# Kernel tuning notes

Measured on AMD Instinct MI355X. Metric: run time of the kernel, lower is better.

The kernel has to match this reference:

```python
import jax, jax.numpy as jnp
import numpy as np
import math

D_MODEL = 1024
HEADS = 16
D_K = D_MODEL // HEADS
D_FF = 2048
EPS = 1e-6
NEG = -1e9


def _layernorm(x, gamma, beta):
    mu = x.mean(axis=-1, keepdims=True)
    var = ((x - mu) ** 2).mean(axis=-1, keepdims=True)
    return gamma * (x - mu) / jnp.sqrt(var + EPS) + beta


def setup_inputs() -> dict:
    key = jax.random.key(0)
    ks = jax.random.split(key, 12)
    B, S = 8, 1024
    s = 0.02
    return {
        "x": jax.random.normal(ks[0], (B, S, D_MODEL), jnp.float32),
        "mask": jnp.ones((B, 1, S), jnp.int32),
        "wq": jax.random.normal(ks[1], (D_MODEL, D_MODEL), jnp.float32) * s,
        "bq": jnp.zeros((D_MODEL,), jnp.float32),
        "wk": jax.random.normal(ks[2], (D_MODEL, D_MODEL), jnp.float32) * s,
        "bk": jnp.zeros((D_MODEL,), jnp.float32),
        "wv": jax.random.normal(ks[3], (D_MODEL, D_MODEL), jnp.float32) * s,
        "bv": jnp.zeros((D_MODEL,), jnp.float32),
        "wo": jax.random.normal(ks[4], (D_MODEL, D_MODEL), jnp.float32) * s,
        "bo": jnp.zeros((D_MODEL,), jnp.float32),
        "w1": jax.random.normal(ks[5], (D_MODEL, D_FF), jnp.float32) * s,
        "b1": jnp.zeros((D_FF,), jnp.float32),
        "w2": jax.random.normal(ks[6], (D_FF, D_MODEL), jnp.float32) * s,
        "b2": jnp.zeros((D_MODEL,), jnp.float32),
        "g1": jnp.ones((D_MODEL,), jnp.float32),
        "be1": jnp.zeros((D_MODEL,), jnp.float32),
        "g2": jnp.ones((D_MODEL,), jnp.float32),
        "be2": jnp.zeros((D_MODEL,), jnp.float32),
    }


def reference(x, mask, wq, bq, wk, bk, wv, bv, wo, bo, w1, b1, w2, b2, g1, be1, g2, be2):
    B, S, _ = x.shape
    # QKV projections, split heads: [B,H,S,d_k]
    q = (x @ wq + bq).reshape(B, S, HEADS, D_K).transpose(0, 2, 1, 3)
    k = (x @ wk + bk).reshape(B, S, HEADS, D_K).transpose(0, 2, 1, 3)
    v = (x @ wv + bv).reshape(B, S, HEADS, D_K).transpose(0, 2, 1, 3)
    scores = jnp.einsum("bhqd,bhkd->bhqk", q, k) / math.sqrt(D_K)
    m = mask[:, None, :, :]  # [B,1,1|S,S] broadcast over heads
    scores = jnp.where(m == 0, NEG, scores)
    attn = jax.nn.softmax(scores, axis=-1)
    out = jnp.einsum("bhqk,bhkd->bhqd", attn, v)
    concat = out.transpose(0, 2, 1, 3).reshape(B, S, D_MODEL)
    attn_out = concat @ wo + bo
    x1 = _layernorm(x + attn_out, g1, be1)
    ff = jax.nn.relu(x1 @ w1 + b1) @ w2 + b2
    return _layernorm(x1 + ff, g2, be2)
```

## Files before the change

### kernel.cpp

```cpp
#include <hip/hip_runtime.h>
#include <stdint.h>

using u16 = unsigned short;
using u32 = unsigned int;
typedef __attribute__((ext_vector_type(4))) float f32x4;
typedef __attribute__((ext_vector_type(8))) short s16x8;

#define LOG2E 1.44269504088896340736f
#define SCL (0.125f * LOG2E)

__device__ __forceinline__ u16 f2b(float f) {
  union { float f; u32 u; } v; v.f = f;
  u32 r = v.u + 0x7fffu + ((v.u >> 16) & 1u);
  return (u16)(r >> 16);
}

__device__ __forceinline__ float b2f(u16 x) {
  union { u32 u; float f; } v; v.u = (u32)x << 16; return v.f;
}

__device__ __forceinline__ u32 pack2(u16 lo, u16 hi) {
  return (u32)lo | ((u32)hi << 16);
}

__device__ __forceinline__ u32 cvtpk(float lo, float hi) {
  u32 r;
  asm("v_cvt_pk_bf16_f32 %0, %1, %2" : "=v"(r) : "v"(lo), "v"(hi));
  return r;
}

__device__ __forceinline__ f32x4 mfma16(s16x8 a, s16x8 b, f32x4 c) {
  return __builtin_amdgcn_mfma_f32_16x16x32_bf16(a, b, c, 0, 0, 0);
}

__device__ __forceinline__ void gload16(const void* g, void* l) {
  __builtin_amdgcn_global_load_lds(
      (const __attribute__((address_space(1))) void*)g,
      (__attribute__((address_space(3))) void*)l, 16, 0, 0);
}

__global__ __launch_bounds__(256) void cvt_bf16(const float* __restrict__ in,
                                                u16* __restrict__ out, int n4) {
  int i = blockIdx.x * 256 + threadIdx.x;
  if (i >= n4) return;
  float4 v = ((const float4*)in)[i];
  uint2 o;
  o.x = pack2(f2b(v.x), f2b(v.y));
  o.y = pack2(f2b(v.z), f2b(v.w));
  ((uint2*)out)[i] = o;
}

__global__ __launch_bounds__(256) void transpose_cvt(const float* __restrict__ in,
                                                     u16* __restrict__ outT,
                                                     int K, int N) {
  __shared__ float t[32][33];
  int n0 = blockIdx.x * 32, k0 = blockIdx.y * 32;
  int tx = threadIdx.x, ty = threadIdx.y;
#pragma unroll
  for (int i = 0; i < 4; i++)
    t[ty + i * 8][tx] = in[(size_t)(k0 + ty + i * 8) * N + n0 + tx];
  __syncthreads();
#pragma unroll
  for (int i = 0; i < 4; i++)
    outT[(size_t)(n0 + ty + i * 8) * K + k0 + tx] = f2b(t[tx][ty + i * 8]);
}

__global__ __launch_bounds__(256) void bias_pack(const float* __restrict__ bq,
                                                 const float* __restrict__ bk,
                                                 const float* __restrict__ bv,
                                                 float* __restrict__ o) {
  int i = blockIdx.x * 256 + threadIdx.x;
  o[i] = (i < 1024) ? bq[i] : (i < 2048) ? bk[i - 1024] : bv[i - 2048];
}

template <int EPI, int BN, int WM, int WN>
__global__ __launch_bounds__(512, 1) void gemm8(const u16* __restrict__ A,
                                                const u16* __restrict__ Bt,
                                                const float* __restrict__ bias,
                                                void* __restrict__ outp,
                                                void* __restrict__ outp2,
                                                int N, int K) {
  constexpr int MI = 256 / (WM * 16);
  constexpr int NJ = BN / (WN * 16);
  constexpr int BB = BN / 128;
  __shared__ u16 As[4][256 * 32];
  __shared__ u16 Bs[4][BN * 32];
  int tid = threadIdx.x;
  int wv = tid >> 6, ln = tid & 63;
  int fr = ln & 15, fg = ln >> 4;
  int wm = wv / WN, wn = wv % WN;

  int x = blockIdx.x & 7;
  int l = blockIdx.x >> 3;
  int m0 = (x * 4 + (l & 3)) * 256;
  int n0 = (l >> 2) * BN;

  auto stageA = [&](int buf, int kt) {
#pragma unroll
    for (int s = 0; s < 2; s++) {
      int idx = s * 512 + tid;
      int row = idx >> 2, ch = idx & 3;
      int sw = (row ^ (row >> 2)) & 3;
      int gcol = kt * 32 + ((ch ^ sw) << 3);
      gload16(A + (size_t)(m0 + row) * K + gcol,
              &As[buf][(size_t)(s * 512 + (wv << 6)) * 8]);
    }
  };
  auto stageB = [&](int buf, int kt) {
#pragma unroll
    for (int s = 0; s < BB; s++) {
      int idx = s * 512 + tid;
      int row = idx >> 2, ch = idx & 3;
      int sw = (row ^ (row >> 2)) & 3;
      int gcol = kt * 32 + ((ch ^ sw) << 3);
      gload16(Bt + (size_t)(n0 + row) * K + gcol,
              &Bs[buf][(size_t)(s * 512 + (wv << 6)) * 8]);
    }
  };

  f32x4 acc[MI][NJ] = {};
  int NT = K >> 5;

#pragma unroll
  for (int tt = 0; tt < 3; ++tt) { stageA(tt, tt); stageB(tt, tt); }

  for (int t = 0; t < NT; ++t) {
    if constexpr (BN == 256) asm volatile("s_waitcnt vmcnt(8)" ::: "memory");
    else                     asm volatile("s_waitcnt vmcnt(6)" ::: "memory");
    __builtin_amdgcn_s_barrier();
    __builtin_amdgcn_sched_barrier(0);

    const u16* Ab = As[t & 3];
    const u16* Bb = Bs[t & 3];
    s16x8 af[MI], bf[NJ];
#pragma unroll
    for (int j = 0; j < NJ; j++) {
      int row = wn * (BN / WN) + j * 16 + fr;
      int sw = (row ^ (row >> 2)) & 3;
      bf[j] = *(const s16x8*)&Bb[row * 32 + ((fg ^ sw) << 3)];
    }
#pragma unroll
    for (int i = 0; i < MI; i++) {
      int row = wm * (256 / WM) + i * 16 + fr;
      int sw = (row ^ (row >> 2)) & 3;
      af[i] = *(const s16x8*)&Ab[row * 32 + ((fg ^ sw) << 3)];
    }

    int tn = (t + 3 < NT) ? t + 3 : NT - 1;
    stageA((t + 3) & 3, tn);
    stageB((t + 3) & 3, tn);

    __builtin_amdgcn_sched_barrier(0);
    __builtin_amdgcn_s_setprio(1);
#pragma unroll
    for (int i = 0; i < MI; i++)
#pragma unroll
      for (int j = 0; j < NJ; j++)
        acc[i][j] = mfma16(af[i], bf[j], acc[i][j]);
    __builtin_amdgcn_s_setprio(0);
    __builtin_amdgcn_sched_barrier(0);
  }

#pragma unroll
  for (int j = 0; j < NJ; j++) {
    int coll = n0 + wn * (BN / WN) + j * 16 + fr;
    float bv = bias[coll];
#pragma unroll
    for (int i = 0; i < MI; i++) {
      int rowbase = m0 + wm * (256 / WM) + i * 16 + fg * 4;
      if (EPI == 4) {
        if (coll < 2048) {
          u16* o = (u16*)outp + (size_t)(coll >> 10) * (8192u * 1024u) + (coll & 1023);
#pragma unroll
          for (int r = 0; r < 4; r++)
            o[(size_t)(rowbase + r) * 1024] = f2b(acc[i][j][r] + bv);
        } else {
          int cv = coll - 2048;
          int b_ = rowbase >> 10, s_ = rowbase & 1023;
          int h_ = cv >> 6, d_ = cv & 63;
          float v0 = acc[i][j][0] + bv, v1 = acc[i][j][1] + bv;
          float v2 = acc[i][j][2] + bv, v3 = acc[i][j][3] + bv;
          uint2 o; o.x = pack2(f2b(v0), f2b(v1)); o.y = pack2(f2b(v2), f2b(v3));
          *(uint2*)((u16*)outp2 + (((size_t)((b_ * 16 + h_) * 64 + d_)) << 10) + s_) = o;
        }
      } else {
#pragma unroll
        for (int r = 0; r < 4; r++) {
          int row = rowbase + r;
          float v = acc[i][j][r] + bv;
          if (EPI == 2) v = v > 0.f ? v : 0.f;
          if (EPI == 1)
            ((float*)outp)[(size_t)row * N + coll] = v;
          else
            ((u16*)outp)[(size_t)row * N + coll] = f2b(v);
        }
      }
    }
  }
}

__global__ __launch_bounds__(256) void attn_fwd(const u16* __restrict__ q,
                                                const u16* __restrict__ k,
                                                const u16* __restrict__ vT,
                                                const int* __restrict__ mask,
                                                u16* __restrict__ ctx) {
  __shared__ u16 Ks[64 * 64];
  __shared__ u16 Vs[2][64 * 64];
  __shared__ u16 Ps[4][32 * 64];
  int tid = threadIdx.x, wv = tid >> 6, ln = tid & 63;
  int fr = ln & 15, fg = ln >> 4;
  int bh = blockIdx.x, b = bh >> 4, h = bh & 15;
  int q0 = blockIdx.y * 128;

  const u16* kbase = k + (size_t)b * 1024 * 1024 + h * 64;
  const u16* vbase = vT + (size_t)bh * 64 * 1024;
#define STAGE_K(kt)                                                           \
  {                                                                           \
    _Pragma("unroll") for (int j = 0; j < 2; j++) {                           \
      int c = wv * 64 + j * 256, cl = c + ln;                                 \
      int rr = cl >> 3, csw = (cl & 7) ^ (rr & 7);                            \
      gload16(kbase + (size_t)((kt) * 64 + rr) * 1024 + csw * 8, Ks + c * 8); \
    }                                                                         \
  }
#define STAGE_V(buf, kt)                                                      \
  {                                                                           \
    _Pragma("unroll") for (int j = 0; j < 2; j++) {                           \
      int c = wv * 64 + j * 256, cl = c + ln;                                 \
      int rr = cl >> 3, csw = (cl & 7) ^ (rr & 7);                            \
      gload16(vbase + (size_t)rr * 1024 + (kt) * 64 + csw * 8,                \
              Vs[buf] + c * 8);                                               \
    }                                                                         \
  }

  STAGE_K(0);
  STAGE_V(0, 0);

  int4 mv0 = *(const int4*)(mask + b * 1024 + tid * 4);
  int ok = (mv0.x != 0) & (mv0.y != 0) & (mv0.z != 0) & (mv0.w != 0);
  int seq_ok = __syncthreads_and(ok);

  s16x8 qf[2][2];
#pragma unroll
  for (int i = 0; i < 2; i++)
#pragma unroll
    for (int ks = 0; ks < 2; ks++) {
      int row = q0 + wv * 32 + i * 16 + fr;
      qf[i][ks] = *(const s16x8*)(q + (size_t)(b * 1024 + row) * 1024 + h * 64 + ks * 32 + fg * 8);
      u32* qw = (u32*)&qf[i][ks];
#pragma unroll
      for (int w = 0; w < 4; w++) {
        union { u32 u; float f; } lo, hi;
        lo.u = qw[w] << 16; hi.u = qw[w] & 0xffff0000u;
        qw[w] = cvtpk(lo.f * SCL, hi.f * SCL);
      }
    }

  s16x8 ones;
#pragma unroll
  for (int j = 0; j < 8; j++) ones[j] = (short)0x3F80;

  f32x4 ao[2][4] = {};
  f32x4 aol[2] = {};
  float mrun[2];
  mrun[0] = mrun[1] = -1e30f;

  int bsrc = (ln & 48) | ((ln >> 2) & 12);

  __syncthreads();

  for (int kt = 0; kt < 16; ++kt) {
    int cur = kt & 1;

    f32x4 st[4][2] = {};
    __builtin_amdgcn_s_setprio(1);
#pragma unroll
    for (int ks = 0; ks < 2; ks++)
#pragma unroll
      for (int jm = 0; jm < 4; jm++) {
        s16x8 kfr = *(const s16x8*)(Ks + (jm * 16 + fr) * 64 + (((ks * 4 + fg) ^ (fr & 7)) << 3));
        st[jm][0] = mfma16(kfr, qf[0][ks], st[jm][0]);
        st[jm][1] = mfma16(kfr, qf[1][ks], st[jm][1]);
      }
    __builtin_amdgcn_s_setprio(0);

    __syncthreads();
    if (kt < 15) {
      STAGE_K(kt + 1);
      STAGE_V(cur ^ 1, kt + 1);
    }

    if (!seq_ok) {
#pragma unroll
      for (int jm = 0; jm < 4; jm++) {
        int4 mv = *(const int4*)(mask + b * 1024 + kt * 64 + jm * 16 + fg * 4);
        float m0 = mv.x == 0 ? -1e9f * SCL : 0.f;
        float m1 = mv.y == 0 ? -1e9f * SCL : 0.f;
        float m2 = mv.z == 0 ? -1e9f * SCL : 0.f;
        float m3 = mv.w == 0 ? -1e9f * SCL : 0.f;
#pragma unroll
        for (int i = 0; i < 2; i++) {
          st[jm][i][0] += m0; st[jm][i][1] += m1;
          st[jm][i][2] += m2; st[jm][i][3] += m3;
        }
      }
    }

    float mx[2];
#pragma unroll
    for (int i = 0; i < 2; i++) {
      float m = fmaxf(fmaxf(st[0][i][0], st[0][i][1]), st[0][i][2]);
      m = fmaxf(fmaxf(m, st[0][i][3]), st[1][i][0]);
      m = fmaxf(fmaxf(m, st[1][i][1]), st[1][i][2]);
      m = fmaxf(fmaxf(m, st[1][i][3]), st[2][i][0]);
      m = fmaxf(fmaxf(m, st[2][i][1]), st[2][i][2]);
      m = fmaxf(fmaxf(m, st[2][i][3]), st[3][i][0]);
      m = fmaxf(fmaxf(m, st[3][i][1]), st[3][i][2]);
      m = fmaxf(m, st[3][i][3]);
      m = fmaxf(m, __shfl_xor(m, 16));
      m = fmaxf(m, __shfl_xor(m, 32));
      mx[i] = m;
    }

    bool need = (mx[0] > mrun[0] + 8.f) || (mx[1] > mrun[1] + 8.f);
    if (__any(need)) {
      float al[2];
#pragma unroll
      for (int i = 0; i < 2; i++) {
        float mnew = fmaxf(mrun[i], mx[i]);
        al[i] = __builtin_exp2f(mrun[i] - mnew);
        mrun[i] = mnew;
      }
#pragma unroll
      for (int io = 0; io < 2; io++) {
        float a0 = __shfl(al[io], bsrc + 0), a1 = __shfl(al[io], bsrc + 1);
        float a2 = __shfl(al[io], bsrc + 2), a3 = __shfl(al[io], bsrc + 3);
        aol[io][0] *= a0; aol[io][1] *= a1; aol[io][2] *= a2; aol[io][3] *= a3;
#pragma unroll
        for (int jd = 0; jd < 4; jd++) {
          ao[io][jd][0] *= a0; ao[io][jd][1] *= a1;
          ao[io][jd][2] *= a2; ao[io][jd][3] *= a3;
        }
      }
    }

#pragma unroll
    for (int i = 0; i < 2; i++)
#pragma unroll
      for (int jm = 0; jm < 4; jm++)
#pragma unroll
        for (int r = 0; r < 4; r++)
          st[jm][i][r] = __builtin_exp2f(st[jm][i][r] - mrun[i]);

    u16* Pw = Ps[wv];
#pragma unroll
    for (int i = 0; i < 2; i++) {
      int qrow = i * 16 + fr;
      int rowoff = qrow * 64;
      int sw = (qrow & 7) << 3;
#pragma unroll
      for (int jm = 0; jm < 4; jm++) {
        uint2 pk;
        pk.x = cvtpk(st[jm][i][0], st[jm][i][1]);
        pk.y = cvtpk(st[jm][i][2], st[jm][i][3]);
        *(uint2*)(Pw + ((rowoff + jm * 16 + fg * 4) ^ sw)) = pk;
      }
    }

    const u16* Vc = Vs[cur];
    __builtin_amdgcn_s_setprio(1);
#pragma unroll
    for (int ks = 0; ks < 2; ks++) {
      int ch = ((ks * 4 + fg) ^ (fr & 7)) << 3;
      s16x8 pa0 = *(const s16x8*)(Pw + fr * 64 + ch);
      s16x8 pa1 = *(const s16x8*)(Pw + (16 + fr) * 64 + ch);
#pragma unroll
      for (int jd = 0; jd < 4; jd++) {
        s16x8 bv = *(const s16x8*)(Vc + (jd * 16 + fr) * 64 + ch);
        ao[0][jd] = mfma16(pa0, bv, ao[0][jd]);
        ao[1][jd] = mfma16(pa1, bv, ao[1][jd]);
      }
      aol[0] = mfma16(pa0, ones, aol[0]);
      aol[1] = mfma16(pa1, ones, aol[1]);
    }
    __builtin_amdgcn_s_setprio(0);

    __syncthreads();
  }

#pragma unroll
  for (int io = 0; io < 2; io++) {
    float i0 = 1.f / aol[io][0], i1 = 1.f / aol[io][1];
    float i2 = 1.f / aol[io][2], i3 = 1.f / aol[io][3];
#pragma unroll
    for (int jd = 0; jd < 4; jd++) {
      int d = jd * 16 + fr;
      int rowb = wv * 32 + io * 16 + fg * 4;
      u16* cb = ctx + (size_t)(b * 1024 + q0 + rowb) * 1024 + h * 64 + d;
      cb[0]    = f2b(ao[io][jd][0] * i0);
      cb[1024] = f2b(ao[io][jd][1] * i1);
      cb[2048] = f2b(ao[io][jd][2] * i2);
      cb[3072] = f2b(ao[io][jd][3] * i3);
    }
  }
#undef STAGE_K
#undef STAGE_V
}

template <bool ABF16, bool BBF16>
__global__ __launch_bounds__(256) void ln_fused(const void* __restrict__ a,
                                                const void* __restrict__ bsrc,
                                                const float* __restrict__ gamma,
                                                const float* __restrict__ beta,
                                                float* __restrict__ outf,
                                                u16* __restrict__ outb) {
  int row = blockIdx.x, tid = threadIdx.x;
  float v0, v1, v2, v3;
  if (ABF16) {
    uint2 va = ((const uint2*)((const u16*)a + (size_t)row * 1024))[tid];
    v0 = b2f((u16)(va.x & 0xffff)); v1 = b2f((u16)(va.x >> 16));
    v2 = b2f((u16)(va.y & 0xffff)); v3 = b2f((u16)(va.y >> 16));
  } else {
    float4 va = ((const float4*)((const float*)a + (size_t)row * 1024))[tid];
    v0 = va.x; v1 = va.y; v2 = va.z; v3 = va.w;
  }
  if (BBF16) {
    uint2 vb = ((const uint2*)((const u16*)bsrc + (size_t)row * 1024))[tid];
    v0 += b2f((u16)(vb.x & 0xffff)); v1 += b2f((u16)(vb.x >> 16));
    v2 += b2f((u16)(vb.y & 0xffff)); v3 += b2f((u16)(vb.y >> 16));
  } else {
    float4 vb = ((const float4*)((const float*)bsrc + (size_t)row * 1024))[tid];
    v0 += vb.x; v1 += vb.y; v2 += vb.z; v3 += vb.w;
  }
  float s = v0 + v1 + v2 + v3;
  float ss = v0 * v0 + v1 * v1 + v2 * v2 + v3 * v3;
#pragma unroll
  for (int m = 1; m < 64; m <<= 1) { s += __shfl_xor(s, m); ss += __shfl_xor(ss, m); }
  __shared__ float rs[8];
  int wv = tid >> 6;
  if ((tid & 63) == 0) { rs[wv] = s; rs[4 + wv] = ss; }
  __syncthreads();
  s = rs[0] + rs[1] + rs[2] + rs[3];
  ss = rs[4] + rs[5] + rs[6] + rs[7];
  float mu = s * (1.f / 1024.f);
  float var = ss * (1.f / 1024.f) - mu * mu;
  float rstd = rsqrtf(var + 1e-6f);
  float4 g4 = ((const float4*)gamma)[tid];
  float4 be4 = ((const float4*)beta)[tid];
  float y0 = g4.x * (v0 - mu) * rstd + be4.x;
  float y1 = g4.y * (v1 - mu) * rstd + be4.y;
  float y2 = g4.z * (v2 - mu) * rstd + be4.z;
  float y3 = g4.w * (v3 - mu) * rstd + be4.w;
  if (outf) {
    float4 o; o.x = y0; o.y = y1; o.z = y2; o.w = y3;
    ((float4*)(outf + (size_t)row * 1024))[tid] = o;
  }
  if (outb) {
    uint2 ob; ob.x = pack2(f2b(y0), f2b(y1)); ob.y = pack2(f2b(y2), f2b(y3));
    ((uint2*)(outb + (size_t)row * 1024))[tid] = ob;
  }
}

extern "C" void kernel_launch(void* const* d_in, const int* in_sizes, int n_in,
                              void* d_out, int out_size, void* d_ws, size_t ws_size,
                              hipStream_t stream) {
  const float* x   = (const float*)d_in[0];
  const int*   msk = (const int*)d_in[1];
  const float* wq  = (const float*)d_in[2];
  const float* bq  = (const float*)d_in[3];
  const float* wk  = (const float*)d_in[4];
  const float* bk  = (const float*)d_in[5];
  const float* wv  = (const float*)d_in[6];
  const float* bv  = (const float*)d_in[7];
  const float* wo  = (const float*)d_in[8];
  const float* bo  = (const float*)d_in[9];
  const float* w1  = (const float*)d_in[10];
  const float* b1  = (const float*)d_in[11];
  const float* w2  = (const float*)d_in[12];
  const float* b2  = (const float*)d_in[13];
  const float* g1  = (const float*)d_in[14];
  const float* be1 = (const float*)d_in[15];
  const float* g2  = (const float*)d_in[16];
  const float* be2 = (const float*)d_in[17];
  float* out = (float*)d_out;
  char* ws = (char*)d_ws;
  const size_t MB = 1u << 20;

  u16* xb  = (u16*)(ws + 0);
  u16* wqt = (u16*)(ws + 16 * MB);
  u16* wkt = (u16*)(ws + 18 * MB);
  u16* wvt = (u16*)(ws + 20 * MB);
  u16* wot = (u16*)(ws + 22 * MB);
  u16* w1t = (u16*)(ws + 24 * MB);
  u16* w2t = (u16*)(ws + 28 * MB);
  u16* qb  = (u16*)(ws + 32 * MB);
  u16* kb  = (u16*)(ws + 48 * MB);
  u16* vT  = (u16*)(ws + 64 * MB);
  u16* ctx = (u16*)(ws + 80 * MB);
  float* bqkv = (float*)(ws + 80 * MB);
  u16* attn_out = (u16*)(ws + 32 * MB);
  u16* x1b = (u16*)(ws + 0);
  u16* hb  = (u16*)(ws + 96 * MB);
  u16* fff = (u16*)(ws + 48 * MB);

  dim3 tb(32, 8);
  cvt_bf16<<<8192, 256, 0, stream>>>(x, xb, 8192 * 1024 / 4);
  transpose_cvt<<<dim3(32, 32), tb, 0, stream>>>(wq, wqt, 1024, 1024);
  transpose_cvt<<<dim3(32, 32), tb, 0, stream>>>(wk, wkt, 1024, 1024);
  transpose_cvt<<<dim3(32, 32), tb, 0, stream>>>(wv, wvt, 1024, 1024);
  transpose_cvt<<<dim3(32, 32), tb, 0, stream>>>(wo, wot, 1024, 1024);
  transpose_cvt<<<dim3(64, 32), tb, 0, stream>>>(w1, w1t, 1024, 2048);
  transpose_cvt<<<dim3(32, 64), tb, 0, stream>>>(w2, w2t, 2048, 1024);
  bias_pack<<<12, 256, 0, stream>>>(bq, bk, bv, bqkv);

  gemm8<4, 256, 2, 4><<<384, 512, 0, stream>>>(xb, wqt, bqkv, qb, vT, 3072, 1024);

  attn_fwd<<<dim3(128, 8), 256, 0, stream>>>(qb, kb, vT, msk, ctx);

  gemm8<0, 128, 4, 2><<<256, 512, 0, stream>>>(ctx, wot, bo, attn_out, nullptr, 1024, 1024);
  ln_fused<false, true><<<8192, 256, 0, stream>>>(x, attn_out, g1, be1, nullptr, x1b);
  gemm8<2, 256, 2, 4><<<256, 512, 0, stream>>>(x1b, w1t, b1, hb, nullptr, 2048, 1024);
  gemm8<0, 128, 4, 2><<<256, 512, 0, stream>>>(hb, w2t, b2, fff, nullptr, 1024, 2048);
  ln_fused<true, true><<<8192, 256, 0, stream>>>(x1b, fff, g2, be2, out, nullptr);
}
```

Measured before the change: 306.8 us.

## Add 256x256 BK64 ping-pong GEMM for QK and FFN1, split V projection

Adds a new GEMM kernel that uses 256x256 tiles, a K-step of 64, double-buffered LDS and XOR-swizzled loads, and issues the next tile's global loads while MFMAs run on four sub-blocks. It replaces the fused QKV GEMM with this kernel for Q and K, plus a separate gemm8 launch for V with a transposed epilogue, and it also takes over the FFN1 ReLU GEMM. The aim is higher MFMA utilisation through larger per-wave tiles and overlapped loads. The costs are an extra kernel launch, the loss of the single fused QKV launch, and high register pressure from 32 accumulators per wave.

```diff
diff --git a/kernel.cpp b/kernel.cpp
--- a/kernel.cpp
+++ b/kernel.cpp
@@ -67,10 +67,134 @@
 
 __global__ __launch_bounds__(256) void bias_pack(const float* __restrict__ bq,
                                                  const float* __restrict__ bk,
-                                                 const float* __restrict__ bv,
                                                  float* __restrict__ o) {
   int i = blockIdx.x * 256 + threadIdx.x;
-  o[i] = (i < 1024) ? bq[i] : (i < 2048) ? bk[i - 1024] : bv[i - 2048];
+  o[i] = (i < 1024) ? bq[i] : bk[i - 1024];
+}
+
+template <int EPI>
+__global__ __launch_bounds__(512, 1) void gemmhk(const u16* __restrict__ A,
+                                                 const u16* __restrict__ Bt,
+                                                 const float* __restrict__ bias,
+                                                 void* __restrict__ outp,
+                                                 int N, int K) {
+  __shared__ u16 As[2][2][128 * 64];
+  __shared__ u16 Bs[2][2][128 * 64];
+  int tid = threadIdx.x;
+  int wv = tid >> 6, ln = tid & 63;
+  int fr = ln & 15, fg = ln >> 4;
+  int wm = wv >> 2, wn = wv & 3;
+
+  int x = blockIdx.x & 7;
+  int l = blockIdx.x >> 3;
+  int m0 = (x * 4 + (l & 3)) * 256;
+  int n0 = (l >> 2) * 256;
+
+  const u16* Abase = A + (size_t)m0 * K;
+  const u16* Bbase = Bt + (size_t)n0 * K;
+
+  auto stage = [&](const u16* gbase, u16* lbase, int kt) {
+#pragma unroll
+    for (int rnd = 0; rnd < 2; rnd++) {
+      int idx = rnd * 512 + tid;
+      int row = idx >> 3, ch = idx & 7;
+      int csw = ch ^ (row & 7);
+      gload16(gbase + (size_t)row * K + kt * 64 + csw * 8,
+              lbase + (size_t)(rnd * 512 + (wv << 6)) * 8);
+    }
+  };
+
+  f32x4 acc[8][4] = {};
+  int NT = K >> 6;
+
+  stage(Abase, &As[0][0][0], 0);
+  stage(Abase + (size_t)128 * K, &As[0][1][0], 0);
+  stage(Bbase, &Bs[0][0][0], 0);
+  stage(Bbase + (size_t)128 * K, &Bs[0][1][0], 0);
+  asm volatile("s_waitcnt vmcnt(0)" ::: "memory");
+  __builtin_amdgcn_s_barrier();
+  __builtin_amdgcn_sched_barrier(0);
+
+  for (int t = 0; t < NT; ++t) {
+    int buf = t & 1, nbuf = buf ^ 1;
+    const u16* Ah = &As[buf][wm][0];
+    const u16* Bh = &Bs[buf][wn >> 1][0];
+    int colb = (wn & 1) * 64;
+    s16x8 a[4][2], b[2][2];
+
+#pragma unroll
+    for (int p = 0; p < 4; p++) {
+      constexpr int PMASK = 1;
+      int mh = p >> 1, nh = p & PMASK;
+      if (nh == 0) {
+#pragma unroll
+        for (int q = 0; q < 4; q++) {
+          int row = mh * 64 + q * 16 + fr;
+#pragma unroll
+          for (int ks = 0; ks < 2; ks++) {
+            int ch = (ks * 4 + fg) ^ (row & 7);
+            a[q][ks] = *(const s16x8*)(Ah + row * 64 + ch * 8);
+          }
+        }
+      }
+#pragma unroll
+      for (int pj = 0; pj < 2; pj++) {
+        int row = colb + nh * 32 + pj * 16 + fr;
+#pragma unroll
+        for (int ks = 0; ks < 2; ks++) {
+          int ch = (ks * 4 + fg) ^ (row & 7);
+          b[pj][ks] = *(const s16x8*)(Bh + row * 64 + ch * 8);
+        }
+      }
+      if (p == 0) {
+        int tn = (t + 1 < NT) ? t + 1 : t;
+        stage(Abase, &As[nbuf][0][0], tn);
+        stage(Abase + (size_t)128 * K, &As[nbuf][1][0], tn);
+        stage(Bbase, &Bs[nbuf][0][0], tn);
+        stage(Bbase + (size_t)128 * K, &Bs[nbuf][1][0], tn);
+      }
+      __builtin_amdgcn_sched_barrier(0);
+      __builtin_amdgcn_s_barrier();
+      __builtin_amdgcn_s_setprio(1);
+#pragma unroll
+      for (int q = 0; q < 4; q++)
+#pragma unroll
+        for (int pj = 0; pj < 2; pj++) {
+          acc[mh * 4 + q][nh * 2 + pj] =
+              mfma16(a[q][0], b[pj][0], acc[mh * 4 + q][nh * 2 + pj]);
+          acc[mh * 4 + q][nh * 2 + pj] =
+              mfma16(a[q][1], b[pj][1], acc[mh * 4 + q][nh * 2 + pj]);
+        }
+      __builtin_amdgcn_s_setprio(0);
+      __builtin_amdgcn_sched_barrier(0);
+    }
+    asm volatile("s_waitcnt vmcnt(0)" ::: "memory");
+    __builtin_amdgcn_s_barrier();
+    __builtin_amdgcn_sched_barrier(0);
+  }
+
+#pragma unroll
+  for (int j = 0; j < 4; j++) {
+    int coll = n0 + wn * 64 + j * 16 + fr;
+    float bv = bias[coll];
+#pragma unroll
+    for (int i = 0; i < 8; i++) {
+      int rowbase = m0 + wm * 128 + i * 16 + fg * 4;
+      if (EPI == 5) {
+        u16* o = (u16*)outp + (size_t)(coll >> 10) * (8192u * 1024u) + (coll & 1023);
+#pragma unroll
+        for (int r = 0; r < 4; r++)
+          o[(size_t)(rowbase + r) * 1024] = f2b(acc[i][j][r] + bv);
+      } else {
+#pragma unroll
+        for (int r = 0; r < 4; r++) {
+          float v = acc[i][j][r] + bv;
+          if (EPI == 2) v = v > 0.f ? v : 0.f;
+          ((u16*)outp)[(size_t)(rowbase + r) * N + coll] = f2b(v);
+        }
+      }
+    }
+  }
 }
 
 template <int EPI, int BN, int WM, int WN>
@@ -78,7 +202,6 @@
                                                 const u16* __restrict__ Bt,
                                                 const float* __restrict__ bias,
                                                 void* __restrict__ outp,
-                                                void* __restrict__ outp2,
                                                 int N, int K) {
   constexpr int MI = 256 / (WM * 16);
   constexpr int NJ = BN / (WN * 16);
@@ -168,31 +291,19 @@
 #pragma unroll
     for (int i = 0; i < MI; i++) {
       int rowbase = m0 + wm * (256 / WM) + i * 16 + fg * 4;
-      if (EPI == 4) {
-        if (coll < 2048) {
-          u16* o = (u16*)outp + (size_t)(coll >> 10) * (8192u * 1024u) + (coll & 1023);
-#pragma unroll
-          for (int r = 0; r < 4; r++)
-            o[(size_t)(rowbase + r) * 1024] = f2b(acc[i][j][r] + bv);
-        } else {
-          int cv = coll - 2048;
-          int b_ = rowbase >> 10, s_ = rowbase & 1023;
-          int h_ = cv >> 6, d_ = cv & 63;
-          float v0 = acc[i][j][0] + bv, v1 = acc[i][j][1] + bv;
-          float v2 = acc[i][j][2] + bv, v3 = acc[i][j][3] + bv;
-          uint2 o; o.x = pack2(f2b(v0), f2b(v1)); o.y = pack2(f2b(v2), f2b(v3));
-          *(uint2*)((u16*)outp2 + (((size_t)((b_ * 16 + h_) * 64 + d_)) << 10) + s_) = o;
-        }
+      if (EPI == 3) {
+        int b_ = rowbase >> 10, s_ = rowbase & 1023;
+        int h_ = coll >> 6, d_ = coll & 63;
+        float v0 = acc[i][j][0] + bv, v1 = acc[i][j][1] + bv;
+        float v2 = acc[i][j][2] + bv, v3 = acc[i][j][3] + bv;
+        uint2 o; o.x = pack2(f2b(v0), f2b(v1)); o.y = pack2(f2b(v2), f2b(v3));
+        *(uint2*)((u16*)outp + (((size_t)((b_ * 16 + h_) * 64 + d_)) << 10) + s_) = o;
       } else {
 #pragma unroll
         for (int r = 0; r < 4; r++) {
           int row = rowbase + r;
           float v = acc[i][j][r] + bv;
-          if (EPI == 2) v = v > 0.f ? v : 0.f;
-          if (EPI == 1)
-            ((float*)outp)[(size_t)row * N + coll] = v;
-          else
-            ((u16*)outp)[(size_t)row * N + coll] = f2b(v);
+          ((u16*)outp)[(size_t)row * N + coll] = f2b(v);
         }
       }
     }
@@ -496,7 +607,7 @@
   u16* kb  = (u16*)(ws + 48 * MB);
   u16* vT  = (u16*)(ws + 64 * MB);
   u16* ctx = (u16*)(ws + 80 * MB);
-  float* bqkv = (float*)(ws + 80 * MB);
+  float* bqk = (float*)(ws + 80 * MB);
   u16* attn_out = (u16*)(ws + 32 * MB);
   u16* x1b = (u16*)(ws + 0);
   u16* hb  = (u16*)(ws + 96 * MB);
@@ -510,15 +621,16 @@
   transpose_cvt<<<dim3(32, 32), tb, 0, stream>>>(wo, wot, 1024, 1024);
   transpose_cvt<<<dim3(64, 32), tb, 0, stream>>>(w1, w1t, 1024, 2048);
   transpose_cvt<<<dim3(32, 64), tb, 0, stream>>>(w2, w2t, 2048, 1024);
-  bias_pack<<<12, 256, 0, stream>>>(bq, bk, bv, bqkv);
-
-  gemm8<4, 256, 2, 4><<<384, 512, 0, stream>>>(xb, wqt, bqkv, qb, vT, 3072, 1024);
+  bias_pack<<<8, 256, 0, stream>>>(bq, bk, bqk);
+
+  gemmhk<5><<<256, 512, 0, stream>>>(xb, wqt, bqk, qb, 2048, 1024);
+  gemm8<3, 128, 4, 2><<<256, 512, 0, stream>>>(xb, wvt, bv, vT, 1024, 1024);
 
   attn_fwd<<<dim3(128, 8), 256, 0, stream>>>(qb, kb, vT, msk, ctx);
 
-  gemm8<0, 128, 4, 2><<<256, 512, 0, stream>>>(ctx, wot, bo, attn_out, nullptr, 1024, 1024);
+  gemm8<0, 128, 4, 2><<<256, 512, 0, stream>>>(ctx, wot, bo, attn_out, 1024, 1024);
   ln_fused<false, true><<<8192, 256, 0, stream>>>(x, attn_out, g1, be1, nullptr, x1b);
-  gemm8<2, 256, 2, 4><<<256, 512, 0, stream>>>(x1b, w1t, b1, hb, nullptr, 2048, 1024);
-  gemm8<0, 128, 4, 2><<<256, 512, 0, stream>>>(hb, w2t, b2, fff, nullptr, 1024, 2048);
+  gemmhk<2><<<256, 512, 0, stream>>>(x1b, w1t, b1, hb, 2048, 1024);
+  gemm8<0, 128, 4, 2><<<256, 512, 0, stream>>>(hb, w2t, b2, fff, 1024, 2048);
   ln_fused<true, true><<<8192, 256, 0, stream>>>(x1b, fff, g2, be2, out, nullptr);
 }
```

Result: faster. 300.2 us (-2.2%).
